# Kernel tuning notes

Measured on AMD Instinct MI355X. Metric: run time of the kernel, lower is better.

The kernel has to match this reference:

```python
import jax, jax.numpy as jnp
import numpy as np

N, C, D_EMB = 4096, 8192, 512
SCALE = 3.0
KL_WEIGHT = 0.2


def _l2norm(x):
    # matches torch F.normalize(p=2, dim=-1) with eps clamp
    return x / jnp.maximum(jnp.linalg.norm(x, axis=-1, keepdims=True), 1e-12)


def setup_inputs() -> dict:
    key = jax.random.key(0)
    k1, k2, k3, k4 = jax.random.split(key, 4)
    X = jax.random.normal(k1, (N, D_EMB), dtype=jnp.float32)
    indices = jax.random.randint(k2, (N,), 0, N)
    T = jax.random.randint(k3, (N,), 0, C)
    proxies = jax.random.normal(k4, (C, D_EMB), dtype=jnp.float32) / 8.0
    sigmas_inv = jnp.full((C, D_EMB), np.log(np.e - 1.0), dtype=jnp.float32)
    return {"X": X, "indices": indices, "T": T, "proxies": proxies, "sigmas_inv": sigmas_inv}


def reference(X, indices, T, proxies, sigmas_inv):
    # per-class diagonal inverse-covariance weights s[c, d] = softplus(sigmas_inv)^2
    s = jax.nn.softplus(sigmas_inv) ** 2                        # (C, D)
    P = SCALE * _l2norm(proxies)                                # (C, D)
    Xn = SCALE * _l2norm(X)                                     # (N, D)
    # Mahalanobis-style distance D[n,c] = sum_d (x_nd - p_cd)^2 * s_cd
    Dmat = (Xn * Xn) @ s.T - 2.0 * (Xn @ (P * s).T) + jnp.sum(P * P * s, axis=-1)[None, :]  # (N, C)
    # log(softmax(-D)) == log_softmax(-D); one-hot targets (smoothing_const=0)
    logp = jax.nn.log_softmax(-Dmat, axis=-1)                   # (N, C)
    ce = -jnp.mean(logp[jnp.arange(Dmat.shape[0]), T])
    # KL regularizer: Sigma = 1/s, mu = normalized proxies
    Sig = 1.0 / s
    mus2 = _l2norm(proxies) ** 2
    kl = jnp.mean(jnp.sum(0.5 * (Sig + mus2 - 1.0 - jnp.log(Sig)), axis=-1))
    return ce + KL_WEIGHT * kl
```

## Files before the change

kernel.cpp:

```cpp
#include <hip/hip_runtime.h>
#include <hip/hip_bf16.h>
#include <cstdint>

#define N_ROWS 4096
#define N_CLS  8192
#define D_EMB  512
#define K_DIM  1024

using f32x4 = __attribute__((ext_vector_type(4))) float;

__device__ __forceinline__ float softplus_f(float v) {
  return (v > 20.f) ? v : log1pf(expf(v));
}

__device__ __forceinline__ unsigned short pack2_e4m3(float a, float b) {
  return (unsigned short)(__builtin_amdgcn_cvt_pk_fp8_f32(a, b, 0, false) & 0xffff);
}

__device__ __forceinline__ float e4m3_to_f(unsigned char v) {
  int e = (v >> 3) & 15, m = v & 7;
  float f;
  if (e) f = __uint_as_float((unsigned int)((e + 120) << 23) | ((unsigned int)m << 20));
  else   f = (float)m * 0.001953125f;
  return (v & 0x80) ? -f : f;
}

__device__ __forceinline__ float block_sum256(float v) {
  __shared__ float red[4];
  #pragma unroll
  for (int o = 32; o; o >>= 1) v += __shfl_xor(v, o);
  __syncthreads();
  if ((threadIdx.x & 63) == 0) red[threadIdx.x >> 6] = v;
  __syncthreads();
  return red[0] + red[1] + red[2] + red[3];
}

__device__ __forceinline__ void global_to_lds16(const void* g, void* l) {
  const __attribute__((address_space(1))) unsigned int* gp =
      reinterpret_cast<const __attribute__((address_space(1))) unsigned int*>(
          reinterpret_cast<uintptr_t>(g));
  __attribute__((address_space(3))) unsigned int* lp =
      reinterpret_cast<__attribute__((address_space(3))) unsigned int*>(
          reinterpret_cast<uintptr_t>(l));
  __builtin_amdgcn_global_load_lds(gp, lp, 16, 0, 0);
}

__global__ __launch_bounds__(256) void k_proxy(const float* __restrict__ proxies,
                                               const float* __restrict__ sigmas_inv,
                                               unsigned char* __restrict__ Bmat,
                                               float* __restrict__ tvec,
                                               float* __restrict__ klc) {
  const int c = blockIdx.x;
  const int tid = threadIdx.x;
  const float* p  = proxies    + (size_t)c * D_EMB;
  const float* si = sigmas_inv + (size_t)c * D_EMB;
  float2 p2 = ((const float2*)p)[tid];
  float ss = block_sum256(p2.x * p2.x + p2.y * p2.y);
  float invn = 1.0f / fmaxf(sqrtf(ss), 1e-12f);
  float2 s2 = ((const float2*)si)[tid];
  float sp0 = softplus_f(s2.x), sp1 = softplus_f(s2.y);
  float s0 = sp0 * sp0, s1 = sp1 * sp1;
  float pn0 = p2.x * invn, pn1 = p2.y * invn;
  float P0 = 3.0f * pn0, P1 = 3.0f * pn1;
  unsigned short* brow = (unsigned short*)(Bmat + (size_t)c * K_DIM);
  brow[tid]       = pack2_e4m3(s0, s1);
  brow[256 + tid] = pack2_e4m3(P0 * s0, P1 * s1);
  float tc = P0 * P0 * s0 + P1 * P1 * s1;
  float kl = 0.5f * (1.0f / s0 + pn0 * pn0 - 1.0f + 2.0f * logf(sp0))
           + 0.5f * (1.0f / s1 + pn1 * pn1 - 1.0f + 2.0f * logf(sp1));
  tc = block_sum256(tc);
  kl = block_sum256(kl);
  if (tid == 0) { tvec[c] = tc; klc[c] = kl; }
}

__global__ __launch_bounds__(256) void k_xprep(const float* __restrict__ X,
                                               unsigned char* __restrict__ Amat) {
  const int n = blockIdx.x;
  const int tid = threadIdx.x;
  const float* x = X + (size_t)n * D_EMB;
  float2 x2 = ((const float2*)x)[tid];
  float ss = block_sum256(x2.x * x2.x + x2.y * x2.y);
  float invn = 3.0f / fmaxf(sqrtf(ss), 1e-12f);
  float v0 = x2.x * invn, v1 = x2.y * invn;
  unsigned short* arow = (unsigned short*)(Amat + (size_t)n * K_DIM);
  arow[tid]       = pack2_e4m3(-v0 * v0, -v1 * v1);
  arow[256 + tid] = pack2_e4m3(2.0f * v0, 2.0f * v1);
}

__global__ __launch_bounds__(512, 4) void k_gemm_lse(const unsigned char* __restrict__ Amat,
                                                     const unsigned char* __restrict__ Bmat,
                                                     const float* __restrict__ tvec,
                                                     float* __restrict__ Pm,
                                                     float* __restrict__ Psum) {
  __shared__ __align__(16) unsigned char lds[73728];
  const int tid  = threadIdx.x;
  const int lane = tid & 63;
  const int wave = tid >> 6;
  const int wr = wave >> 1, wc = wave & 1;
  const int swz  = ((int)blockIdx.x & 7) * 128 + ((int)blockIdx.x >> 3);
  const int rt   = swz & 15;
  const int ct   = swz >> 4;
  const int row0 = rt * 256;
  const int col0 = ct * 128;

  f32x4 acc[4][4];
  #pragma unroll
  for (int i = 0; i < 4; ++i)
    #pragma unroll
    for (int j = 0; j < 4; ++j) acc[i][j] = (f32x4){0.f, 0.f, 0.f, 0.f};

  const int arow = wr * 64 + (lane & 15);
  const int bcol = wc * 64 + (lane & 15);
  const int kb8  = (lane >> 4) * 8;

  int offA[4][2], offB[4][2];
  #pragma unroll
  for (int mi = 0; mi < 4; ++mi) {
    #pragma unroll
    for (int s2 = 0; s2 < 2; ++s2) {
      int f = (arow + mi * 16) * 64 + kb8 + s2 * 32;
      offA[mi][s2] = f ^ (((f >> 7) & 7) << 4);
      int g = (bcol + mi * 16) * 64 + kb8 + s2 * 32;
      offB[mi][s2] = g ^ (((g >> 7) & 7) << 4);
    }
  }
  const int f0 = tid * 16;
  const int f1 = 8192 + tid * 16;
  const int sf0 = f0 ^ (((f0 >> 7) & 7) << 4);
  const int sf1 = f1 ^ (((f1 >> 7) & 7) << 4);
  const unsigned char* gA0 = Amat + (size_t)(row0 + (sf0 >> 6)) * K_DIM + (sf0 & 63);
  const unsigned char* gA1 = Amat + (size_t)(row0 + (sf1 >> 6)) * K_DIM + (sf1 & 63);
  const unsigned char* gB0 = Bmat + (size_t)(col0 + (sf0 >> 6)) * K_DIM + (sf0 & 63);

  auto stg = [&](int slot, int ko) {
    global_to_lds16(gA0 + ko, lds + slot * 16384 + f0);
    global_to_lds16(gA1 + ko, lds + slot * 16384 + f1);
    global_to_lds16(gB0 + ko, lds + 49152 + slot * 8192 + f0);
  };
  auto compute = [&](int sa, int sb) {
    __builtin_amdgcn_s_setprio(1);
    #pragma unroll
    for (int s2 = 0; s2 < 2; ++s2) {
      long a[4], b[4];
      #pragma unroll
      for (int mi = 0; mi < 4; ++mi) a[mi] = *(const long*)(lds + sa + offA[mi][s2]);
      #pragma unroll
      for (int ni = 0; ni < 4; ++ni) b[ni] = *(const long*)(lds + sb + offB[ni][s2]);
      #pragma unroll
      for (int mi = 0; mi < 4; ++mi)
        #pragma unroll
        for (int ni = 0; ni < 4; ++ni)
          acc[mi][ni] = __builtin_amdgcn_mfma_f32_16x16x32_fp8_fp8(a[mi], b[ni], acc[mi][ni], 0, 0, 0);
    }
    __builtin_amdgcn_s_setprio(0);
  };

  stg(0, 0);
  stg(1, 64);
#define GITER(T, NW) \
  __builtin_amdgcn_s_barrier(); \
  if ((T) + 2 < 16) stg(((T) + 2) % 3, ((T) + 2) * 64); \
  asm volatile("s_waitcnt vmcnt(" #NW ")" ::: "memory"); \
  __builtin_amdgcn_sched_barrier(0); \
  __builtin_amdgcn_s_barrier(); \
  compute(((T) % 3) * 16384, 49152 + ((T) % 3) * 8192);

  GITER(0, 6)  GITER(1, 6)  GITER(2, 6)  GITER(3, 6)
  GITER(4, 6)  GITER(5, 6)  GITER(6, 6)  GITER(7, 6)
  GITER(8, 6)  GITER(9, 6)  GITER(10, 6) GITER(11, 6)
  GITER(12, 6) GITER(13, 6) GITER(14, 3) GITER(15, 0)
#undef GITER

  float (*ms)[2][2] = (float (*)[2][2])(lds + 16384);
  float tc[4];
  #pragma unroll
  for (int ni = 0; ni < 4; ++ni)
    tc[ni] = tvec[col0 + wc * 64 + ni * 16 + (lane & 15)];

  #pragma unroll
  for (int mi = 0; mi < 4; ++mi) {
    #pragma unroll
    for (int j = 0; j < 4; ++j) {
      float z0 = acc[mi][0][j] - tc[0];
      float z1 = acc[mi][1][j] - tc[1];
      float z2 = acc[mi][2][j] - tc[2];
      float z3 = acc[mi][3][j] - tc[3];
      float m = fmaxf(fmaxf(z0, z1), fmaxf(z2, z3));
      #pragma unroll
      for (int o = 1; o < 16; o <<= 1) m = fmaxf(m, __shfl_xor(m, o));
      float s = __expf(z0 - m) + __expf(z1 - m) + __expf(z2 - m) + __expf(z3 - m);
      #pragma unroll
      for (int o = 1; o < 16; o <<= 1) s += __shfl_xor(s, o);
      if ((lane & 15) == 0) {
        int rloc = wr * 64 + mi * 16 + ((lane >> 4) << 2) + j;
        ms[rloc][wc][0] = m;
        ms[rloc][wc][1] = s;
      }
    }
  }
  __syncthreads();
  if (tid < 256) {
    float m0 = ms[tid][0][0], s0 = ms[tid][0][1];
    float m1 = ms[tid][1][0], s1 = ms[tid][1][1];
    float M = fmaxf(m0, m1);
    float S = s0 * __expf(m0 - M) + s1 * __expf(m1 - M);
    Pm  [(size_t)(row0 + tid) * 64 + ct] = M;
    Psum[(size_t)(row0 + tid) * 64 + ct] = S;
  }
}

__global__ __launch_bounds__(256) void k_target(const unsigned char* __restrict__ Amat,
                                                const unsigned char* __restrict__ Bmat,
                                                const float* __restrict__ tvec,
                                                const int* __restrict__ T,
                                                float* __restrict__ tgt) {
  const int lane = threadIdx.x & 63;
  const int n = blockIdx.x * 4 + (threadIdx.x >> 6);
  const int c = T[n];
  uint4 av = *(const uint4*)(Amat + (size_t)n * K_DIM + lane * 16);
  uint4 bv = *(const uint4*)(Bmat + (size_t)c * K_DIM + lane * 16);
  const unsigned char* ab = (const unsigned char*)&av;
  const unsigned char* bb = (const unsigned char*)&bv;
  float s = 0.f;
  #pragma unroll
  for (int i = 0; i < 16; ++i) s += e4m3_to_f(ab[i]) * e4m3_to_f(bb[i]);
  #pragma unroll
  for (int o = 32; o; o >>= 1) s += __shfl_xor(s, o);
  if (lane == 0) tgt[n] = s - tvec[c];
}

__global__ __launch_bounds__(256) void k_red(const float* __restrict__ Pm,
                                             const float* __restrict__ Psum,
                                             const float* __restrict__ tgt,
                                             const float* __restrict__ klc,
                                             float* __restrict__ cep,
                                             float* __restrict__ klp) {
  const int b = blockIdx.x;
  const int tid = threadIdx.x;
  const int n = b * 16 + (tid >> 4);
  const int l4 = tid & 15;
  float4 pm = *(const float4*)(Pm   + (size_t)n * 64 + l4 * 4);
  float4 ps = *(const float4*)(Psum + (size_t)n * 64 + l4 * 4);
  float m = fmaxf(fmaxf(pm.x, pm.y), fmaxf(pm.z, pm.w));
  #pragma unroll
  for (int o = 1; o < 16; o <<= 1) m = fmaxf(m, __shfl_xor(m, o));
  float S = ps.x * __expf(pm.x - m) + ps.y * __expf(pm.y - m)
          + ps.z * __expf(pm.z - m) + ps.w * __expf(pm.w - m);
  #pragma unroll
  for (int o = 1; o < 16; o <<= 1) S += __shfl_xor(S, o);
  float ce = (l4 == 0) ? (m + logf(S) - tgt[n]) : 0.f;
  float kl = (tid < 32) ? klc[b * 32 + tid] : 0.f;
  ce = block_sum256(ce);
  kl = block_sum256(kl);
  if (tid == 0) { cep[b] = ce; klp[b] = kl; }
}

__global__ __launch_bounds__(256) void k_fin2(const float* __restrict__ cep,
                                              const float* __restrict__ klp,
                                              float* __restrict__ out) {
  const int tid = threadIdx.x;
  float ce = block_sum256(cep[tid]);
  float kl = block_sum256(klp[tid]);
  if (tid == 0) out[0] = ce / (float)N_ROWS + 0.2f * (kl / (float)N_CLS);
}

extern "C" void kernel_launch(void* const* d_in, const int* in_sizes, int n_in,
                              void* d_out, int out_size, void* d_ws, size_t ws_size,
                              hipStream_t stream) {
  const float* X          = (const float*)d_in[0];
  const int*   T          = (const int*)d_in[2];
  const float* proxies    = (const float*)d_in[3];
  const float* sigmas_inv = (const float*)d_in[4];

  char* ws = (char*)d_ws;
  unsigned char* Amat = (unsigned char*)ws;
  unsigned char* Bmat = (unsigned char*)(ws + (4u << 20));
  float* tvec = (float*)(ws + (12u << 20));
  float* klc  = (float*)(ws + (12u << 20) + (32u << 10));
  float* Pm   = (float*)(ws + (12u << 20) + (64u << 10));
  float* Psum = (float*)(ws + (13u << 20) + (64u << 10));
  float* tgt  = (float*)(ws + (14u << 20) + (64u << 10));
  float* cep  = (float*)(ws + (14u << 20) + (80u << 10));
  float* klp  = (float*)(ws + (14u << 20) + (84u << 10));
  float* out  = (float*)d_out;

  hipLaunchKernelGGL(k_proxy,    dim3(N_CLS),      dim3(256), 0, stream, proxies, sigmas_inv, Bmat, tvec, klc);
  hipLaunchKernelGGL(k_xprep,    dim3(N_ROWS),     dim3(256), 0, stream, X, Amat);
  hipLaunchKernelGGL(k_gemm_lse, dim3(1024),       dim3(512), 0, stream, Amat, Bmat, tvec, Pm, Psum);
  hipLaunchKernelGGL(k_target,   dim3(N_ROWS / 4), dim3(256), 0, stream, Amat, Bmat, tvec, T, tgt);
  hipLaunchKernelGGL(k_red,      dim3(256),        dim3(256), 0, stream, Pm, Psum, tgt, klc, cep, klp);
  hipLaunchKernelGGL(k_fin2,     dim3(1),          dim3(256), 0, stream, cep, klp, out);
}
```

Baseline: 92.42 us.

## Merge prep kernels, fold target dot into reduction, shrink GEMM tile to 128x128

Combines the proxy and X preparation kernels into one launch and folds the per-row target logit computation into the final reduction kernel, removing two launches and a global round trip. The GEMM tile drops from 256x128 with 512 threads and a triple-buffered hand-scheduled pipeline to 128x128 with 256 threads, a simple double buffer and __syncthreads. The smaller LDS footprint and a 5-block occupancy hint are meant to fit more blocks per CU. The trade-off is less data reuse per block and loss of the explicit vmcnt-based overlap, and the global_load_lds writes may not be waited on before the barrier.

```diff
diff --git a/kernel.cpp b/kernel.cpp
--- a/kernel.cpp
+++ b/kernel.cpp
@@ -45,62 +45,63 @@
   __builtin_amdgcn_global_load_lds(gp, lp, 16, 0, 0);
 }
 
-__global__ __launch_bounds__(256) void k_proxy(const float* __restrict__ proxies,
-                                               const float* __restrict__ sigmas_inv,
-                                               unsigned char* __restrict__ Bmat,
-                                               float* __restrict__ tvec,
-                                               float* __restrict__ klc) {
-  const int c = blockIdx.x;
+__global__ __launch_bounds__(256) void k_prep(const float* __restrict__ proxies,
+                                              const float* __restrict__ sigmas_inv,
+                                              const float* __restrict__ X,
+                                              unsigned char* __restrict__ Bmat,
+                                              unsigned char* __restrict__ Amat,
+                                              float* __restrict__ tvec,
+                                              float* __restrict__ klc) {
+  const int bid = blockIdx.x;
   const int tid = threadIdx.x;
-  const float* p  = proxies    + (size_t)c * D_EMB;
-  const float* si = sigmas_inv + (size_t)c * D_EMB;
-  float2 p2 = ((const float2*)p)[tid];
-  float ss = block_sum256(p2.x * p2.x + p2.y * p2.y);
-  float invn = 1.0f / fmaxf(sqrtf(ss), 1e-12f);
-  float2 s2 = ((const float2*)si)[tid];
-  float sp0 = softplus_f(s2.x), sp1 = softplus_f(s2.y);
-  float s0 = sp0 * sp0, s1 = sp1 * sp1;
-  float pn0 = p2.x * invn, pn1 = p2.y * invn;
-  float P0 = 3.0f * pn0, P1 = 3.0f * pn1;
-  unsigned short* brow = (unsigned short*)(Bmat + (size_t)c * K_DIM);
-  brow[tid]       = pack2_e4m3(s0, s1);
-  brow[256 + tid] = pack2_e4m3(P0 * s0, P1 * s1);
-  float tc = P0 * P0 * s0 + P1 * P1 * s1;
-  float kl = 0.5f * (1.0f / s0 + pn0 * pn0 - 1.0f + 2.0f * logf(sp0))
-           + 0.5f * (1.0f / s1 + pn1 * pn1 - 1.0f + 2.0f * logf(sp1));
-  tc = block_sum256(tc);
-  kl = block_sum256(kl);
-  if (tid == 0) { tvec[c] = tc; klc[c] = kl; }
-}
-
-__global__ __launch_bounds__(256) void k_xprep(const float* __restrict__ X,
-                                               unsigned char* __restrict__ Amat) {
-  const int n = blockIdx.x;
-  const int tid = threadIdx.x;
-  const float* x = X + (size_t)n * D_EMB;
-  float2 x2 = ((const float2*)x)[tid];
-  float ss = block_sum256(x2.x * x2.x + x2.y * x2.y);
-  float invn = 3.0f / fmaxf(sqrtf(ss), 1e-12f);
-  float v0 = x2.x * invn, v1 = x2.y * invn;
-  unsigned short* arow = (unsigned short*)(Amat + (size_t)n * K_DIM);
-  arow[tid]       = pack2_e4m3(-v0 * v0, -v1 * v1);
-  arow[256 + tid] = pack2_e4m3(2.0f * v0, 2.0f * v1);
-}
-
-__global__ __launch_bounds__(512, 4) void k_gemm_lse(const unsigned char* __restrict__ Amat,
+  if (bid < N_CLS) {
+    const int c = bid;
+    const float* p  = proxies    + (size_t)c * D_EMB;
+    const float* si = sigmas_inv + (size_t)c * D_EMB;
+    float2 p2 = ((const float2*)p)[tid];
+    float ss = block_sum256(p2.x * p2.x + p2.y * p2.y);
+    float invn = 1.0f / fmaxf(sqrtf(ss), 1e-12f);
+    float2 s2 = ((const float2*)si)[tid];
+    float sp0 = softplus_f(s2.x), sp1 = softplus_f(s2.y);
+    float s0 = sp0 * sp0, s1 = sp1 * sp1;
+    float pn0 = p2.x * invn, pn1 = p2.y * invn;
+    float P0 = 3.0f * pn0, P1 = 3.0f * pn1;
+    unsigned short* brow = (unsigned short*)(Bmat + (size_t)c * K_DIM);
+    brow[tid]       = pack2_e4m3(s0, s1);
+    brow[256 + tid] = pack2_e4m3(P0 * s0, P1 * s1);
+    float tc = P0 * P0 * s0 + P1 * P1 * s1;
+    float kl = 0.5f * (1.0f / s0 + pn0 * pn0 - 1.0f + 2.0f * logf(sp0))
+             + 0.5f * (1.0f / s1 + pn1 * pn1 - 1.0f + 2.0f * logf(sp1));
+    tc = block_sum256(tc);
+    kl = block_sum256(kl);
+    if (tid == 0) { tvec[c] = tc; klc[c] = kl; }
+  } else {
+    const int n = bid - N_CLS;
+    const float* x = X + (size_t)n * D_EMB;
+    float2 x2 = ((const float2*)x)[tid];
+    float ss = block_sum256(x2.x * x2.x + x2.y * x2.y);
+    float invn = 3.0f / fmaxf(sqrtf(ss), 1e-12f);
+    float v0 = x2.x * invn, v1 = x2.y * invn;
+    unsigned short* arow = (unsigned short*)(Amat + (size_t)n * K_DIM);
+    arow[tid]       = pack2_e4m3(-v0 * v0, -v1 * v1);
+    arow[256 + tid] = pack2_e4m3(2.0f * v0, 2.0f * v1);
+  }
+}
+
+__global__ __launch_bounds__(256, 5) void k_gemm_lse(const unsigned char* __restrict__ Amat,
                                                      const unsigned char* __restrict__ Bmat,
                                                      const float* __restrict__ tvec,
                                                      float* __restrict__ Pm,
                                                      float* __restrict__ Psum) {
-  __shared__ __align__(16) unsigned char lds[73728];
+  __shared__ __align__(16) unsigned char lds[32768];
   const int tid  = threadIdx.x;
   const int lane = tid & 63;
   const int wave = tid >> 6;
   const int wr = wave >> 1, wc = wave & 1;
-  const int swz  = ((int)blockIdx.x & 7) * 128 + ((int)blockIdx.x >> 3);
-  const int rt   = swz & 15;
-  const int ct   = swz >> 4;
-  const int row0 = rt * 256;
+  const int swz  = ((int)blockIdx.x & 7) * 256 + ((int)blockIdx.x >> 3);
+  const int rt   = swz & 31;
+  const int ct   = swz >> 5;
+  const int row0 = rt * 128;
   const int col0 = ct * 128;
 
   f32x4 acc[4][4];
@@ -113,39 +114,42 @@
   const int bcol = wc * 64 + (lane & 15);
   const int kb8  = (lane >> 4) * 8;
 
-  int offA[4][2], offB[4][2];
-  #pragma unroll
-  for (int mi = 0; mi < 4; ++mi) {
-    #pragma unroll
-    for (int s2 = 0; s2 < 2; ++s2) {
-      int f = (arow + mi * 16) * 64 + kb8 + s2 * 32;
-      offA[mi][s2] = f ^ (((f >> 7) & 7) << 4);
-      int g = (bcol + mi * 16) * 64 + kb8 + s2 * 32;
-      offB[mi][s2] = g ^ (((g >> 7) & 7) << 4);
-    }
-  }
-  const int f0 = tid * 16;
-  const int f1 = 8192 + tid * 16;
+  const int f0  = tid * 16;
+  const int f1  = 4096 + tid * 16;
   const int sf0 = f0 ^ (((f0 >> 7) & 7) << 4);
   const int sf1 = f1 ^ (((f1 >> 7) & 7) << 4);
   const unsigned char* gA0 = Amat + (size_t)(row0 + (sf0 >> 6)) * K_DIM + (sf0 & 63);
   const unsigned char* gA1 = Amat + (size_t)(row0 + (sf1 >> 6)) * K_DIM + (sf1 & 63);
   const unsigned char* gB0 = Bmat + (size_t)(col0 + (sf0 >> 6)) * K_DIM + (sf0 & 63);
+  const unsigned char* gB1 = Bmat + (size_t)(col0 + (sf1 >> 6)) * K_DIM + (sf1 & 63);
 
   auto stg = [&](int slot, int ko) {
-    global_to_lds16(gA0 + ko, lds + slot * 16384 + f0);
-    global_to_lds16(gA1 + ko, lds + slot * 16384 + f1);
-    global_to_lds16(gB0 + ko, lds + 49152 + slot * 8192 + f0);
+    unsigned char* la = lds + slot * 8192;
+    unsigned char* lb = lds + 16384 + slot * 8192;
+    global_to_lds16(gA0 + ko, la + f0);
+    global_to_lds16(gA1 + ko, la + f1);
+    global_to_lds16(gB0 + ko, lb + f0);
+    global_to_lds16(gB1 + ko, lb + f1);
   };
-  auto compute = [&](int sa, int sb) {
+  auto ld64 = [&](const unsigned char* base, int row, int kb) -> long {
+    int f = row * 64 + kb;
+    return *(const long*)(base + (f ^ (((f >> 7) & 7) << 4)));
+  };
+
+  stg(0, 0);
+  __syncthreads();
+  for (int t = 0; t < 16; ++t) {
+    if (t < 15) stg((t + 1) & 1, (t + 1) * 64);
+    const unsigned char* Ab = lds + (t & 1) * 8192;
+    const unsigned char* Bb = lds + 16384 + (t & 1) * 8192;
     __builtin_amdgcn_s_setprio(1);
     #pragma unroll
-    for (int s2 = 0; s2 < 2; ++s2) {
+    for (int ks = 0; ks < 64; ks += 32) {
       long a[4], b[4];
       #pragma unroll
-      for (int mi = 0; mi < 4; ++mi) a[mi] = *(const long*)(lds + sa + offA[mi][s2]);
-      #pragma unroll
-      for (int ni = 0; ni < 4; ++ni) b[ni] = *(const long*)(lds + sb + offB[ni][s2]);
+      for (int mi = 0; mi < 4; ++mi) a[mi] = ld64(Ab, arow + mi * 16, ks + kb8);
+      #pragma unroll
+      for (int ni = 0; ni < 4; ++ni) b[ni] = ld64(Bb, bcol + ni * 16, ks + kb8);
       #pragma unroll
       for (int mi = 0; mi < 4; ++mi)
         #pragma unroll
@@ -153,25 +157,10 @@
           acc[mi][ni] = __builtin_amdgcn_mfma_f32_16x16x32_fp8_fp8(a[mi], b[ni], acc[mi][ni], 0, 0, 0);
     }
     __builtin_amdgcn_s_setprio(0);
-  };
-
-  stg(0, 0);
-  stg(1, 64);
-#define GITER(T, NW) \
-  __builtin_amdgcn_s_barrier(); \
-  if ((T) + 2 < 16) stg(((T) + 2) % 3, ((T) + 2) * 64); \
-  asm volatile("s_waitcnt vmcnt(" #NW ")" ::: "memory"); \
-  __builtin_amdgcn_sched_barrier(0); \
-  __builtin_amdgcn_s_barrier(); \
-  compute(((T) % 3) * 16384, 49152 + ((T) % 3) * 8192);
-
-  GITER(0, 6)  GITER(1, 6)  GITER(2, 6)  GITER(3, 6)
-  GITER(4, 6)  GITER(5, 6)  GITER(6, 6)  GITER(7, 6)
-  GITER(8, 6)  GITER(9, 6)  GITER(10, 6) GITER(11, 6)
-  GITER(12, 6) GITER(13, 6) GITER(14, 3) GITER(15, 0)
-#undef GITER
-
-  float (*ms)[2][2] = (float (*)[2][2])(lds + 16384);
+    __syncthreads();
+  }
+
+  float (*ms)[2][2] = (float (*)[2][2])lds;
   float tc[4];
   #pragma unroll
   for (int ni = 0; ni < 4; ++ni)
@@ -199,7 +188,7 @@
     }
   }
   __syncthreads();
-  if (tid < 256) {
+  if (tid < 128) {
     float m0 = ms[tid][0][0], s0 = ms[tid][0][1];
     float m1 = ms[tid][1][0], s1 = ms[tid][1][1];
     float M = fmaxf(m0, m1);
@@ -209,35 +198,39 @@
   }
 }
 
-__global__ __launch_bounds__(256) void k_target(const unsigned char* __restrict__ Amat,
-                                                const unsigned char* __restrict__ Bmat,
-                                                const float* __restrict__ tvec,
-                                                const int* __restrict__ T,
-                                                float* __restrict__ tgt) {
-  const int lane = threadIdx.x & 63;
-  const int n = blockIdx.x * 4 + (threadIdx.x >> 6);
-  const int c = T[n];
-  uint4 av = *(const uint4*)(Amat + (size_t)n * K_DIM + lane * 16);
-  uint4 bv = *(const uint4*)(Bmat + (size_t)c * K_DIM + lane * 16);
-  const unsigned char* ab = (const unsigned char*)&av;
-  const unsigned char* bb = (const unsigned char*)&bv;
-  float s = 0.f;
-  #pragma unroll
-  for (int i = 0; i < 16; ++i) s += e4m3_to_f(ab[i]) * e4m3_to_f(bb[i]);
-  #pragma unroll
-  for (int o = 32; o; o >>= 1) s += __shfl_xor(s, o);
-  if (lane == 0) tgt[n] = s - tvec[c];
-}
-
 __global__ __launch_bounds__(256) void k_red(const float* __restrict__ Pm,
                                              const float* __restrict__ Psum,
-                                             const float* __restrict__ tgt,
+                                             const unsigned char* __restrict__ Amat,
+                                             const unsigned char* __restrict__ Bmat,
+                                             const float* __restrict__ tvec,
+                                             const int* __restrict__ T,
                                              const float* __restrict__ klc,
                                              float* __restrict__ cep,
                                              float* __restrict__ klp) {
+  __shared__ float tgt_s[16];
   const int b = blockIdx.x;
   const int tid = threadIdx.x;
-  const int n = b * 16 + (tid >> 4);
+  const int lane = tid & 63;
+  const int w = tid >> 6;
+  #pragma unroll
+  for (int r = 0; r < 4; ++r) {
+    const int loc = w * 4 + r;
+    const int n = b * 16 + loc;
+    const int c = T[n];
+    uint4 av = *(const uint4*)(Amat + (size_t)n * K_DIM + lane * 16);
+    uint4 bv = *(const uint4*)(Bmat + (size_t)c * K_DIM + lane * 16);
+    const unsigned char* ab = (const unsigned char*)&av;
+    const unsigned char* bb = (const unsigned char*)&bv;
+    float s = 0.f;
+    #pragma unroll
+    for (int i = 0; i < 16; ++i) s += e4m3_to_f(ab[i]) * e4m3_to_f(bb[i]);
+    #pragma unroll
+    for (int o = 32; o; o >>= 1) s += __shfl_xor(s, o);
+    if (lane == 0) tgt_s[loc] = s - tvec[c];
+  }
+  __syncthreads();
+  const int loc = tid >> 4;
+  const int n = b * 16 + loc;
   const int l4 = tid & 15;
   float4 pm = *(const float4*)(Pm   + (size_t)n * 64 + l4 * 4);
   float4 ps = *(const float4*)(Psum + (size_t)n * 64 + l4 * 4);
@@ -248,7 +241,7 @@
           + ps.z * __expf(pm.z - m) + ps.w * __expf(pm.w - m);
   #pragma unroll
   for (int o = 1; o < 16; o <<= 1) S += __shfl_xor(S, o);
-  float ce = (l4 == 0) ? (m + logf(S) - tgt[n]) : 0.f;
+  float ce = (l4 == 0) ? (m + logf(S) - tgt_s[loc]) : 0.f;
   float kl = (tid < 32) ? klc[b * 32 + tid] : 0.f;
   ce = block_sum256(ce);
   kl = block_sum256(kl);
@@ -279,15 +272,16 @@
   float* klc  = (float*)(ws + (12u << 20) + (32u << 10));
   float* Pm   = (float*)(ws + (12u << 20) + (64u << 10));
   float* Psum = (float*)(ws + (13u << 20) + (64u << 10));
-  float* tgt  = (float*)(ws + (14u << 20) + (64u << 10));
-  float* cep  = (float*)(ws + (14u << 20) + (80u << 10));
-  float* klp  = (float*)(ws + (14u << 20) + (84u << 10));
+  float* cep  = (float*)(ws + (14u << 20) + (64u << 10));
+  float* klp  = (float*)(ws + (14u << 20) + (68u << 10));
   float* out  = (float*)d_out;
 
-  hipLaunchKernelGGL(k_proxy,    dim3(N_CLS),      dim3(256), 0, stream, proxies, sigmas_inv, Bmat, tvec, klc);
-  hipLaunchKernelGGL(k_xprep,    dim3(N_ROWS),     dim3(256), 0, stream, X, Amat);
-  hipLaunchKernelGGL(k_gemm_lse, dim3(1024),       dim3(512), 0, stream, Amat, Bmat, tvec, Pm, Psum);
-  hipLaunchKernelGGL(k_target,   dim3(N_ROWS / 4), dim3(256), 0, stream, Amat, Bmat, tvec, T, tgt);
-  hipLaunchKernelGGL(k_red,      dim3(256),        dim3(256), 0, stream, Pm, Psum, tgt, klc, cep, klp);
-  hipLaunchKernelGGL(k_fin2,     dim3(1),          dim3(256), 0, stream, cep, klp, out);
-}
+  hipLaunchKernelGGL(k_prep,     dim3(N_CLS + N_ROWS), dim3(256), 0, stream,
+                     proxies, sigmas_inv, X, Bmat, Amat, tvec, klc);
+  hipLaunchKernelGGL(k_gemm_lse, dim3(2048),           dim3(256), 0, stream,
+                     Amat, Bmat, tvec, Pm, Psum);
+  hipLaunchKernelGGL(k_red,      dim3(256),            dim3(256), 0, stream,
+                     Pm, Psum, Amat, Bmat, tvec, T, klc, cep, klp);
+  hipLaunchKernelGGL(k_fin2,     dim3(1),              dim3(256), 0, stream,
+                     cep, klp, out);
+}
```

Result: slower. 106.0 us (+14.7%).
